# Optimization experiments

Hardware: AMD Instinct MI355X
Metric: run time of the kernel (lower is better)

The kernel has to match this reference:

```python
import jax, jax.numpy as jnp
import numpy as np
import math

N, E, B, T = 100000, 500000, 4096, 12
IN, HID, H = 64, 32, 4
HC = HID * H  # 128
ED = 4


def setup_inputs() -> dict:
    key = jax.random.key(0)
    ks = jax.random.split(key, 40)
    w = lambda k, shape: jax.random.normal(k, shape, jnp.float32) * 0.05
    inp = {
        'x': jax.random.normal(ks[0], (N, IN), jnp.float32),
        'edge_index': jax.random.randint(ks[1], (2, E), 0, N, jnp.int32),
        'edge_attr': jax.random.normal(ks[2], (E, ED), jnp.float32),
        'batch': jnp.sort(jax.random.randint(ks[3], (N,), 0, B, jnp.int32)),
        'r_target': jax.random.randint(ks[4], (B,), 0, T, jnp.int32),
        # layer 1 (in=IN)
        'Wq1': w(ks[5], (IN, HC)), 'bq1': w(ks[6], (HC,)),
        'Wk1': w(ks[7], (IN, HC)), 'bk1': w(ks[8], (HC,)),
        'Wv1': w(ks[9], (IN, HC)), 'bv1': w(ks[10], (HC,)),
        'We1': w(ks[11], (ED, HC)),
        'Ws1': w(ks[12], (IN, HC)), 'bs1': w(ks[13], (HC,)),
        # layers 2 and 3 stacked (in=HC)
        'Wq23': w(ks[14], (2, HC, HC)), 'bq23': w(ks[15], (2, HC)),
        'Wk23': w(ks[16], (2, HC, HC)), 'bk23': w(ks[17], (2, HC)),
        'Wv23': w(ks[18], (2, HC, HC)), 'bv23': w(ks[19], (2, HC)),
        'We23': w(ks[20], (2, ED, HC)),
        'Ws23': w(ks[21], (2, HC, HC)), 'bs23': w(ks[22], (2, HC)),
        # per-task linear heads (out_channels=1)
        'head_W': w(ks[23], (T, HC)), 'head_b': w(ks[24], (T,)),
    }
    return inp


def tconv(x, src, dst, ea, Wq, bq, Wk, bk, Wv, bv, We, Ws, bs):
    """PyG TransformerConv: gather -> per-edge MHA score -> segment softmax -> scatter."""
    q = (x @ Wq + bq).reshape(-1, H, HID)   # [N,H,C]
    k = (x @ Wk + bk).reshape(-1, H, HID)
    v = (x @ Wv + bv).reshape(-1, H, HID)
    e = (ea @ We).reshape(-1, H, HID)       # [E,H,C] (lin_edge has no bias)
    kj = k[src] + e                          # [E,H,C]
    alpha = (q[dst] * kj).sum(-1) / math.sqrt(HID)          # [E,H]
    amax = jax.ops.segment_max(alpha, dst, num_segments=N)  # [N,H]
    alpha = jnp.exp(alpha - amax[dst])
    asum = jax.ops.segment_sum(alpha, dst, num_segments=N)
    alpha = alpha / (asum[dst] + 1e-16)
    msg = (v[src] + e) * alpha[..., None]                   # [E,H,C]
    out = jax.ops.segment_sum(msg, dst, num_segments=N).reshape(N, HC)
    return out + x @ Ws + bs                 # root_weight skip connection


def reference(x, edge_index, edge_attr, batch, r_target,
              Wq1, bq1, Wk1, bk1, Wv1, bv1, We1, Ws1, bs1,
              Wq23, bq23, Wk23, bk23, Wv23, bv23, We23, Ws23, bs23,
              head_W, head_b):
    src, dst = edge_index[0], edge_index[1]
    h = jax.nn.relu(tconv(x, src, dst, edge_attr, Wq1, bq1, Wk1, bk1, Wv1, bv1, We1, Ws1, bs1))
    h = jax.nn.relu(tconv(h, src, dst, edge_attr, Wq23[0], bq23[0], Wk23[0], bk23[0], Wv23[0], bv23[0], We23[0], Ws23[0], bs23[0]))
    h = tconv(h, src, dst, edge_attr, Wq23[1], bq23[1], Wk23[1], bk23[1], Wv23[1], bv23[1], We23[1], Ws23[1], bs23[1])
    # global mean pool per graph
    cnt = jax.ops.segment_sum(jnp.ones((N,), h.dtype), batch, num_segments=B)
    pooled = jax.ops.segment_sum(h, batch, num_segments=B) / jnp.maximum(cnt, 1.0)[:, None]  # [B,HC]
    # dropout p=0.3 is a no-op in eval mode
    # per-task head selected by r_target (out_channels=1, squeezed)
    return (pooled * head_W[r_target]).sum(-1) + head_b[r_target]  # [B]
```

## Files before the change

### kernel.cpp

```cpp
#include <hip/hip_runtime.h>
#include <hip/hip_bf16.h>

#define NN 100000
#define EE 500000
#define BB 4096
#define HC 128
#define SCAN_ELEM 1024
#define NSB ((NN + SCAN_ELEM - 1) / SCAN_ELEM)

typedef __bf16 bf16_t;
typedef bf16_t bf16x8 __attribute__((ext_vector_type(8)));
typedef float f32x4 __attribute__((ext_vector_type(4)));
typedef float f32x2 __attribute__((ext_vector_type(2)));

__device__ __forceinline__ unsigned short f2bf(float f) {
    unsigned u = __builtin_bit_cast(unsigned, f);
    u += 0x7FFFu + ((u >> 16) & 1u);
    return (unsigned short)(u >> 16);
}
__device__ __forceinline__ float bflo(unsigned u) {
    return __builtin_bit_cast(float, u << 16);
}
__device__ __forceinline__ float bfhi(unsigned u) {
    return __builtin_bit_cast(float, u & 0xFFFF0000u);
}
__device__ __forceinline__ f32x2 unpk2(unsigned u) {
    return (f32x2){ bflo(u), bfhi(u) };
}

__global__ __launch_bounds__(256) void prep_w(
    const float* __restrict__ Wq, const float* __restrict__ Wk,
    const float* __restrict__ Wv, const float* __restrict__ Ws,
    unsigned short* __restrict__ Wt, int K)
{
    const int g = blockIdx.x * 256 + threadIdx.x;
    const int per = K * 128;
    if (g >= 4 * per) return;
    const int p = g / per, r = g - p * per;
    const int k = r >> 7, n = r & 127;
    const float* W = p == 0 ? Wq : p == 1 ? Wk : p == 2 ? Wv : Ws;
    Wt[(size_t)p * per + (size_t)n * K + k] = f2bf(W[k * 128 + n]);
}

template<int NKT, int F32A>
__global__ __launch_bounds__(256) void gemm_mfma(
    const unsigned short* __restrict__ Abf,
    const float* __restrict__ xf,
    const unsigned short* __restrict__ Wt,
    const float* __restrict__ bq, const float* __restrict__ bk,
    const float* __restrict__ bv, const float* __restrict__ bs,
    unsigned* __restrict__ QSb, unsigned* __restrict__ KVb)
{
    constexpr int K = NKT * 32;
    const int lane = threadIdx.x & 63;
    const int p = threadIdx.x >> 6;
    const int m = lane & 15, kq = lane >> 4;
    const int rows0 = blockIdx.x * 32;

    const unsigned short* Wp = Wt + (size_t)p * 128 * K;
    const float* bias = p == 0 ? bq : p == 1 ? bk : p == 2 ? bv : bs;

    bf16x8 a[2][NKT];
#pragma unroll
    for (int mt = 0; mt < 2; mt++)
#pragma unroll
        for (int kt = 0; kt < NKT; kt++) {
            if constexpr (F32A) {
                const float* pr = xf + (size_t)(rows0 + mt * 16 + m) * K + kt * 32 + kq * 8;
                const float4 f0 = *(const float4*)pr;
                const float4 f1 = *(const float4*)(pr + 4);
                union { bf16x8 v; unsigned short u8[8]; } cv;
                cv.u8[0] = f2bf(f0.x); cv.u8[1] = f2bf(f0.y);
                cv.u8[2] = f2bf(f0.z); cv.u8[3] = f2bf(f0.w);
                cv.u8[4] = f2bf(f1.x); cv.u8[5] = f2bf(f1.y);
                cv.u8[6] = f2bf(f1.z); cv.u8[7] = f2bf(f1.w);
                a[mt][kt] = cv.v;
            } else {
                a[mt][kt] = *(const bf16x8*)(Abf + (size_t)(rows0 + mt * 16 + m) * K + kt * 32 + kq * 8);
            }
        }

    f32x4 acc[2][8];
#pragma unroll
    for (int mt = 0; mt < 2; mt++)
#pragma unroll
        for (int nt = 0; nt < 8; nt++)
            acc[mt][nt] = (f32x4){0.f, 0.f, 0.f, 0.f};

#pragma unroll
    for (int nt = 0; nt < 8; nt++) {
#pragma unroll
        for (int kt = 0; kt < NKT; kt++) {
            const bf16x8 b = *(const bf16x8*)(Wp + (size_t)(nt * 16 + m) * K + kt * 32 + kq * 8);
            acc[0][nt] = __builtin_amdgcn_mfma_f32_16x16x32_bf16(a[0][kt], b, acc[0][nt], 0, 0, 0);
            acc[1][nt] = __builtin_amdgcn_mfma_f32_16x16x32_bf16(a[1][kt], b, acc[1][nt], 0, 0, 0);
        }
    }

    unsigned* out = p == 0 ? QSb : p == 1 ? KVb : p == 2 ? (KVb + 64) : (QSb + 64);
#pragma unroll
    for (int nt = 0; nt < 8; nt++) {
        const float bi = bias[nt * 16 + m];
#pragma unroll
        for (int mt = 0; mt < 2; mt++) {
#pragma unroll
            for (int r = 0; r < 4; r++) {
                const float v0 = acc[mt][nt][r] + bi;
                const float v1 = __shfl_xor(v0, 1);
                if (!(m & 1)) {
                    const unsigned pk = (unsigned)f2bf(v0) | ((unsigned)f2bf(v1) << 16);
                    out[(size_t)(rows0 + mt * 16 + kq * 4 + r) * 128 + nt * 8 + (m >> 1)] = pk;
                }
            }
        }
    }
}

__global__ __launch_bounds__(256) void deg_k(const int* __restrict__ ei, int* __restrict__ deg)
{
    const int e = blockIdx.x * 256 + threadIdx.x;
    if (e < EE) atomicAdd(&deg[ei[EE + e]], 1);
}

__global__ __launch_bounds__(256) void scan_part(const int* __restrict__ deg,
                                                 int* __restrict__ bsum)
{
    __shared__ int red[256];
    const int base = blockIdx.x * SCAN_ELEM + threadIdx.x * 4;
    int s = 0;
#pragma unroll
    for (int j = 0; j < 4; j++) { const int i = base + j; if (i < NN) s += deg[i]; }
    red[threadIdx.x] = s;
    __syncthreads();
    for (int st = 128; st > 0; st >>= 1) {
        if (threadIdx.x < st) red[threadIdx.x] += red[threadIdx.x + st];
        __syncthreads();
    }
    if (threadIdx.x == 0) bsum[blockIdx.x] = red[0];
}

__global__ __launch_bounds__(128) void scan_top(const int* __restrict__ bsum,
                                                int* __restrict__ boff)
{
    __shared__ int buf[128];
    const int v = (threadIdx.x < NSB) ? bsum[threadIdx.x] : 0;
    buf[threadIdx.x] = v;
    __syncthreads();
    for (int s = 1; s < 128; s <<= 1) {
        const int t = (threadIdx.x >= s) ? buf[threadIdx.x - s] : 0;
        __syncthreads();
        buf[threadIdx.x] += t;
        __syncthreads();
    }
    if (threadIdx.x < NSB) boff[threadIdx.x] = buf[threadIdx.x] - v;
}

__global__ __launch_bounds__(256) void scan_final(const int* __restrict__ deg,
                                                  const int* __restrict__ boff,
                                                  int* __restrict__ off,
                                                  int* __restrict__ cursor)
{
    __shared__ int tsum[256];
    const int base = blockIdx.x * SCAN_ELEM + threadIdx.x * 4;
    int vals[4];
    int s = 0;
#pragma unroll
    for (int j = 0; j < 4; j++) {
        const int i = base + j;
        vals[j] = (i < NN) ? deg[i] : 0;
        s += vals[j];
    }
    tsum[threadIdx.x] = s;
    __syncthreads();
    for (int st = 1; st < 256; st <<= 1) {
        const int t = (threadIdx.x >= st) ? tsum[threadIdx.x - st] : 0;
        __syncthreads();
        tsum[threadIdx.x] += t;
        __syncthreads();
    }
    int ex = boff[blockIdx.x] + tsum[threadIdx.x] - s;
#pragma unroll
    for (int j = 0; j < 4; j++) {
        const int i = base + j;
        if (i < NN) { off[i] = ex; cursor[i] = ex; }
        ex += vals[j];
    }
    if (blockIdx.x == NSB - 1 && threadIdx.x == 255)
        off[NN] = boff[blockIdx.x] + tsum[255];
}

__global__ __launch_bounds__(256) void bucket_k(const int* __restrict__ ei,
                                                const float* __restrict__ ea,
                                                int* __restrict__ cursor,
                                                int* __restrict__ esrc,
                                                float4* __restrict__ eaf)
{
    const int e = blockIdx.x * 256 + threadIdx.x;
    if (e < EE) {
        const int d = ei[EE + e];
        const int p = atomicAdd(&cursor[d], 1);
        esrc[p] = ei[e];
        eaf[p] = *(const float4*)(ea + (size_t)e * 4);
    }
}

__global__ __launch_bounds__(256) void cnt_k(const int* __restrict__ batch,
                                             float* __restrict__ cnt)
{
    const int n = blockIdx.x * 256 + threadIdx.x;
    if (n < NN) atomicAdd(&cnt[batch[n]], 1.0f);
}

__global__ __launch_bounds__(256) void edge_fused(
    const int* __restrict__ esrc, const float4* __restrict__ eaf,
    const float* __restrict__ We,
    const unsigned* __restrict__ QSb, const unsigned* __restrict__ KVb,
    const int* __restrict__ off,
    unsigned short* __restrict__ Hb,
    const int* __restrict__ batch, float* __restrict__ pooled,
    int fuse_pool)
{
    const int lane = threadIdx.x & 63;
    const int slot = lane >> 4;
    const int c8   = lane & 15;
    const int cb   = c8 * 8;
    const int ceq  = cb + slot * 2;
    const int n = blockIdx.x * 4 + (threadIdx.x >> 6);

    const int beg = off[n], end = off[n + 1];

    const uint4 qv = *(const uint4*)(QSb + (size_t)n * 128 + c8 * 4);
    const unsigned sku = QSb[(size_t)n * 128 + 64 + c8 * 4 + slot];
    f32x2 q2[4];
    q2[0] = unpk2(qv.x); q2[1] = unpk2(qv.y);
    q2[2] = unpk2(qv.z); q2[3] = unpk2(qv.w);

    float qep[4];
#pragma unroll
    for (int d = 0; d < 4; d++) {
        const float4 wa = *(const float4*)(We + d * HC + cb);
        const float4 wb = *(const float4*)(We + d * HC + cb + 4);
        qep[d] = wa.x * q2[0].x + wa.y * q2[0].y + wa.z * q2[1].x + wa.w * q2[1].y
               + wb.x * q2[2].x + wb.y * q2[2].y + wb.z * q2[3].x + wb.w * q2[3].y;
    }

    f32x2 num2[4] = {(f32x2){0.f, 0.f}, (f32x2){0.f, 0.f},
                     (f32x2){0.f, 0.f}, (f32x2){0.f, 0.f}};
    f32x4 s4 = (f32x4){0.f, 0.f, 0.f, 0.f};
    float den = 0.f;

    if (beg < end) {
        const int e1 = end - 1;
        int p0 = beg + slot; if (p0 > e1) p0 = e1;
        int src = esrc[p0];
        float4 a4 = eaf[p0];
        for (int base = beg; base < end; base += 4) {
            const unsigned* kv = KVb + (size_t)src * 128 + c8 * 4;
            const uint4 ku = *(const uint4*)kv;
            const uint4 vu = *(const uint4*)(kv + 64);
            const float4 ac = a4;
            const bool act = (base + slot) < end;
            if (base + 4 < end) {
                int pn = base + 4 + slot; if (pn > e1) pn = e1;
                src = esrc[pn]; a4 = eaf[pn];
            }
            f32x2 t2 = q2[0] * unpk2(ku.x);
            t2 += q2[1] * unpk2(ku.y);
            t2 += q2[2] * unpk2(ku.z);
            t2 += q2[3] * unpk2(ku.w);
            float tot = t2.x + t2.y
                      + ac.x * qep[0] + ac.y * qep[1] + ac.z * qep[2] + ac.w * qep[3];
            tot += __shfl_xor(tot, 1);
            tot += __shfl_xor(tot, 2);
            float al = __expf(tot * 0.17677669529663687f);
            if (!act) al = 0.f;
            num2[0] += unpk2(vu.x) * al;
            num2[1] += unpk2(vu.y) * al;
            num2[2] += unpk2(vu.z) * al;
            num2[3] += unpk2(vu.w) * al;
            s4.x += ac.x * al; s4.y += ac.y * al;
            s4.z += ac.z * al; s4.w += ac.w * al;
            den += al;
        }
    }

#pragma unroll
    for (int j = 0; j < 4; j++) {
        num2[j].x += __shfl_xor(num2[j].x, 16);
        num2[j].y += __shfl_xor(num2[j].y, 16);
        num2[j].x += __shfl_xor(num2[j].x, 32);
        num2[j].y += __shfl_xor(num2[j].y, 32);
    }
    s4.x += __shfl_xor(s4.x, 16); s4.y += __shfl_xor(s4.y, 16);
    s4.z += __shfl_xor(s4.z, 16); s4.w += __shfl_xor(s4.w, 16);
    s4.x += __shfl_xor(s4.x, 32); s4.y += __shfl_xor(s4.y, 32);
    s4.z += __shfl_xor(s4.z, 32); s4.w += __shfl_xor(s4.w, 32);
    den += __shfl_xor(den, 16);
    den += __shfl_xor(den, 32);
    const float inv = 1.f / (den + 1e-16f);

    f32x2 mynum = slot == 0 ? num2[0] : slot == 1 ? num2[1]
                : slot == 2 ? num2[2] : num2[3];
    float ev0 = 0.f, ev1 = 0.f;
#pragma unroll
    for (int d = 0; d < 4; d++) {
        const float2 wd = *(const float2*)(We + d * HC + ceq);
        const float sd = d == 0 ? s4.x : d == 1 ? s4.y : d == 2 ? s4.z : s4.w;
        ev0 += sd * wd.x;
        ev1 += sd * wd.y;
    }
    const float o0 = (mynum.x + ev0) * inv + bflo(sku);
    const float o1 = (mynum.y + ev1) * inv + bfhi(sku);

    if (!fuse_pool) {
        const float r0 = fmaxf(o0, 0.f), r1 = fmaxf(o1, 0.f);
        const unsigned pk = (unsigned)f2bf(r0) | ((unsigned)f2bf(r1) << 16);
        *(unsigned*)(Hb + (size_t)n * HC + ceq) = pk;
    } else {
        const int b = batch[n];
        atomicAdd(pooled + (size_t)b * HC + ceq,     o0);
        atomicAdd(pooled + (size_t)b * HC + ceq + 1, o1);
    }
}

__global__ __launch_bounds__(256) void head_k(
    const float* __restrict__ pooled, const float* __restrict__ cnt,
    const int* __restrict__ rt, const float* __restrict__ hW,
    const float* __restrict__ hb, float* __restrict__ out)
{
    const int lane = threadIdx.x & 63;
    const int b = blockIdx.x * 4 + (threadIdx.x >> 6);
    if (b >= BB) return;
    const int t = rt[b];
    const int c = lane * 2;
    const float2 p2 = *(const float2*)(pooled + (size_t)b * HC + c);
    const float2 w2 = *(const float2*)(hW + (size_t)t * HC + c);
    float part = p2.x * w2.x + p2.y * w2.y;
    part += __shfl_xor(part, 1);
    part += __shfl_xor(part, 2);
    part += __shfl_xor(part, 4);
    part += __shfl_xor(part, 8);
    part += __shfl_xor(part, 16);
    part += __shfl_xor(part, 32);
    if (lane == 0) out[b] = part / fmaxf(cnt[b], 1.0f) + hb[t];
}

extern "C" void kernel_launch(void* const* d_in, const int* in_sizes, int n_in,
                              void* d_out, int out_size, void* d_ws, size_t ws_size,
                              hipStream_t stream) {
    const float* x      = (const float*)d_in[0];
    const int*   ei     = (const int*)d_in[1];
    const float* ea     = (const float*)d_in[2];
    const int*   batch  = (const int*)d_in[3];
    const int*   rt     = (const int*)d_in[4];

    unsigned* QSb = (unsigned*)d_ws;
    unsigned* KVb = QSb + 12800000;
    unsigned short* Abf = (unsigned short*)(KVb + 12800000);
    float4* eaf   = (float4*)(Abf + 12800000);
    unsigned short* Wt = (unsigned short*)(eaf + 500000);
    float* pooled = (float*)(Wt + 65536);
    float* cnt    = pooled + 524288;
    int*   esrc   = (int*)(cnt + 4096);
    int*   deg    = esrc + 500000;
    int*   off    = deg + 100000;
    int*   cursor = off + 100004;
    int*   bsum   = cursor + 100000;
    int*   boff   = bsum + 128;

    hipMemsetAsync(deg, 0, 100000 * sizeof(int), stream);
    deg_k<<<(EE + 255) / 256, 256, 0, stream>>>(ei, deg);
    scan_part<<<NSB, 256, 0, stream>>>(deg, bsum);
    scan_top<<<1, 128, 0, stream>>>(bsum, boff);
    scan_final<<<NSB, 256, 0, stream>>>(deg, boff, off, cursor);
    bucket_k<<<(EE + 255) / 256, 256, 0, stream>>>(ei, ea, cursor, esrc, eaf);

    hipMemsetAsync(pooled, 0, (size_t)(BB * HC + BB) * sizeof(float), stream);
    cnt_k<<<(NN + 255) / 256, 256, 0, stream>>>(batch, cnt);

    for (int l = 0; l < 3; l++) {
        const int K = (l == 0) ? 64 : 128;
        const float *Wq, *Wk, *Wv, *Wsk, *bq, *bk, *bv, *bs, *We;
        if (l == 0) {
            Wq = (const float*)d_in[5];  bq = (const float*)d_in[6];
            Wk = (const float*)d_in[7];  bk = (const float*)d_in[8];
            Wv = (const float*)d_in[9];  bv = (const float*)d_in[10];
            We = (const float*)d_in[11];
            Wsk= (const float*)d_in[12]; bs = (const float*)d_in[13];
        } else {
            const int j = l - 1;
            Wq = (const float*)d_in[14] + (size_t)j * HC * HC;  bq = (const float*)d_in[15] + j * HC;
            Wk = (const float*)d_in[16] + (size_t)j * HC * HC;  bk = (const float*)d_in[17] + j * HC;
            Wv = (const float*)d_in[18] + (size_t)j * HC * HC;  bv = (const float*)d_in[19] + j * HC;
            We = (const float*)d_in[20] + (size_t)j * 4 * HC;
            Wsk= (const float*)d_in[21] + (size_t)j * HC * HC;  bs = (const float*)d_in[22] + j * HC;
        }

        prep_w<<<(4 * K * 128 + 255) / 256, 256, 0, stream>>>(Wq, Wk, Wv, Wsk, Wt, K);
        if (K == 64)
            gemm_mfma<2, 1><<<NN / 32, 256, 0, stream>>>(Abf, x, Wt, bq, bk, bv, bs, QSb, KVb);
        else
            gemm_mfma<4, 0><<<NN / 32, 256, 0, stream>>>(Abf, x, Wt, bq, bk, bv, bs, QSb, KVb);
        edge_fused<<<NN / 4, 256, 0, stream>>>(esrc, eaf, We, QSb, KVb, off,
                                               Abf, batch, pooled,
                                               l == 2 ? 1 : 0);
    }

    head_k<<<BB / 4, 256, 0, stream>>>(pooled, cnt, rt,
        (const float*)d_in[23], (const float*)d_in[24], (float*)d_out);
}
```

Before: 664.6 us.

## Batch weight prep, fold count kernel into scan, use packed bf16 converts and nontemporal stores

Converts all three layers' weights to bf16 in one launch instead of one launch per layer. Folds the per-graph node count into scan_final and merges the two memsets into one, so fewer kernels and memsets are launched. Replaces the manual bf16 rounding with the v_cvt_pk_bf16_f32 packed-convert instruction, and writes the GEMM and layer outputs with nontemporal stores. The nontemporal stores may hurt the next kernel, which reads those outputs back soon after.

```diff
diff --git a/kernel.cpp b/kernel.cpp
--- a/kernel.cpp
+++ b/kernel.cpp
@@ -27,19 +27,36 @@
 __device__ __forceinline__ f32x2 unpk2(unsigned u) {
     return (f32x2){ bflo(u), bfhi(u) };
 }
-
-__global__ __launch_bounds__(256) void prep_w(
-    const float* __restrict__ Wq, const float* __restrict__ Wk,
-    const float* __restrict__ Wv, const float* __restrict__ Ws,
-    unsigned short* __restrict__ Wt, int K)
+__device__ __forceinline__ unsigned pkbf(float lo, float hi) {
+    unsigned r;
+    asm volatile("v_cvt_pk_bf16_f32 %0, %1, %2" : "=v"(r) : "v"(lo), "v"(hi));
+    return r;
+}
+
+__global__ __launch_bounds__(256) void prep_w_all(
+    const float* __restrict__ Wq1, const float* __restrict__ Wk1,
+    const float* __restrict__ Wv1, const float* __restrict__ Ws1,
+    const float* __restrict__ Wq23, const float* __restrict__ Wk23,
+    const float* __restrict__ Wv23, const float* __restrict__ Ws23,
+    unsigned short* __restrict__ Wt3)
 {
     const int g = blockIdx.x * 256 + threadIdx.x;
-    const int per = K * 128;
-    if (g >= 4 * per) return;
-    const int p = g / per, r = g - p * per;
-    const int k = r >> 7, n = r & 127;
-    const float* W = p == 0 ? Wq : p == 1 ? Wk : p == 2 ? Wv : Ws;
-    Wt[(size_t)p * per + (size_t)n * K + k] = f2bf(W[k * 128 + n]);
+    if (g >= 32768 + 131072) return;
+    if (g < 32768) {
+        const int p = g >> 13, r = g & 8191;
+        const int k = r >> 7, n = r & 127;
+        const float* W = p == 0 ? Wq1 : p == 1 ? Wk1 : p == 2 ? Wv1 : Ws1;
+        Wt3[p * 8192 + n * 64 + k] = f2bf(W[k * 128 + n]);
+    } else {
+        const int g2 = g - 32768;
+        const int j = g2 >> 16;
+        const int r3 = g2 & 65535;
+        const int p = r3 >> 14, r = r3 & 16383;
+        const int k = r >> 7, n = r & 127;
+        const float* W = (p == 0 ? Wq23 : p == 1 ? Wk23 : p == 2 ? Wv23 : Ws23)
+                       + (size_t)j * 128 * 128;
+        Wt3[65536 + j * 65536 + p * 16384 + n * 128 + k] = f2bf(W[k * 128 + n]);
+    }
 }
 
 template<int NKT, int F32A>
@@ -69,11 +86,11 @@
                 const float* pr = xf + (size_t)(rows0 + mt * 16 + m) * K + kt * 32 + kq * 8;
                 const float4 f0 = *(const float4*)pr;
                 const float4 f1 = *(const float4*)(pr + 4);
-                union { bf16x8 v; unsigned short u8[8]; } cv;
-                cv.u8[0] = f2bf(f0.x); cv.u8[1] = f2bf(f0.y);
-                cv.u8[2] = f2bf(f0.z); cv.u8[3] = f2bf(f0.w);
-                cv.u8[4] = f2bf(f1.x); cv.u8[5] = f2bf(f1.y);
-                cv.u8[6] = f2bf(f1.z); cv.u8[7] = f2bf(f1.w);
+                union { bf16x8 v; unsigned u[4]; } cv;
+                cv.u[0] = pkbf(f0.x, f0.y);
+                cv.u[1] = pkbf(f0.z, f0.w);
+                cv.u[2] = pkbf(f1.x, f1.y);
+                cv.u[3] = pkbf(f1.z, f1.w);
                 a[mt][kt] = cv.v;
             } else {
                 a[mt][kt] = *(const bf16x8*)(Abf + (size_t)(rows0 + mt * 16 + m) * K + kt * 32 + kq * 8);
@@ -108,8 +125,9 @@
                 const float v0 = acc[mt][nt][r] + bi;
                 const float v1 = __shfl_xor(v0, 1);
                 if (!(m & 1)) {
-                    const unsigned pk = (unsigned)f2bf(v0) | ((unsigned)f2bf(v1) << 16);
-                    out[(size_t)(rows0 + mt * 16 + kq * 4 + r) * 128 + nt * 8 + (m >> 1)] = pk;
+                    const unsigned pk = pkbf(v0, v1);
+                    __builtin_nontemporal_store(pk,
+                        &out[(size_t)(rows0 + mt * 16 + kq * 4 + r) * 128 + nt * 8 + (m >> 1)]);
                 }
             }
         }
@@ -158,7 +176,9 @@
 __global__ __launch_bounds__(256) void scan_final(const int* __restrict__ deg,
                                                   const int* __restrict__ boff,
                                                   int* __restrict__ off,
-                                                  int* __restrict__ cursor)
+                                                  int* __restrict__ cursor,
+                                                  const int* __restrict__ batch,
+                                                  float* __restrict__ cnt)
 {
     __shared__ int tsum[256];
     const int base = blockIdx.x * SCAN_ELEM + threadIdx.x * 4;
@@ -182,7 +202,10 @@
 #pragma unroll
     for (int j = 0; j < 4; j++) {
         const int i = base + j;
-        if (i < NN) { off[i] = ex; cursor[i] = ex; }
+        if (i < NN) {
+            off[i] = ex; cursor[i] = ex;
+            atomicAdd(&cnt[batch[i]], 1.0f);
+        }
         ex += vals[j];
     }
     if (blockIdx.x == NSB - 1 && threadIdx.x == 255)
@@ -202,13 +225,6 @@
         esrc[p] = ei[e];
         eaf[p] = *(const float4*)(ea + (size_t)e * 4);
     }
-}
-
-__global__ __launch_bounds__(256) void cnt_k(const int* __restrict__ batch,
-                                             float* __restrict__ cnt)
-{
-    const int n = blockIdx.x * 256 + threadIdx.x;
-    if (n < NN) atomicAdd(&cnt[batch[n]], 1.0f);
 }
 
 __global__ __launch_bounds__(256) void edge_fused(
@@ -313,9 +329,8 @@
     const float o1 = (mynum.y + ev1) * inv + bfhi(sku);
 
     if (!fuse_pool) {
-        const float r0 = fmaxf(o0, 0.f), r1 = fmaxf(o1, 0.f);
-        const unsigned pk = (unsigned)f2bf(r0) | ((unsigned)f2bf(r1) << 16);
-        *(unsigned*)(Hb + (size_t)n * HC + ceq) = pk;
+        const unsigned pk = pkbf(fmaxf(o0, 0.f), fmaxf(o1, 0.f));
+        __builtin_nontemporal_store(pk, (unsigned*)(Hb + (size_t)n * HC + ceq));
     } else {
         const int b = batch[n];
         atomicAdd(pooled + (size_t)b * HC + ceq,     o0);
@@ -358,46 +373,47 @@
     unsigned* KVb = QSb + 12800000;
     unsigned short* Abf = (unsigned short*)(KVb + 12800000);
     float4* eaf   = (float4*)(Abf + 12800000);
-    unsigned short* Wt = (unsigned short*)(eaf + 500000);
-    float* pooled = (float*)(Wt + 65536);
+    unsigned short* Wt3 = (unsigned short*)(eaf + 500000);
+    float* pooled = (float*)(Wt3 + 196608);
     float* cnt    = pooled + 524288;
-    int*   esrc   = (int*)(cnt + 4096);
-    int*   deg    = esrc + 500000;
-    int*   off    = deg + 100000;
+    int*   deg    = (int*)(cnt + 4096);
+    int*   esrc   = deg + 100000;
+    int*   off    = esrc + 500000;
     int*   cursor = off + 100004;
     int*   bsum   = cursor + 100000;
     int*   boff   = bsum + 128;
 
-    hipMemsetAsync(deg, 0, 100000 * sizeof(int), stream);
+    hipMemsetAsync(pooled, 0, (size_t)(524288 + 4096 + 100000) * sizeof(float), stream);
+
     deg_k<<<(EE + 255) / 256, 256, 0, stream>>>(ei, deg);
     scan_part<<<NSB, 256, 0, stream>>>(deg, bsum);
     scan_top<<<1, 128, 0, stream>>>(bsum, boff);
-    scan_final<<<NSB, 256, 0, stream>>>(deg, boff, off, cursor);
+    scan_final<<<NSB, 256, 0, stream>>>(deg, boff, off, cursor, batch, cnt);
     bucket_k<<<(EE + 255) / 256, 256, 0, stream>>>(ei, ea, cursor, esrc, eaf);
 
-    hipMemsetAsync(pooled, 0, (size_t)(BB * HC + BB) * sizeof(float), stream);
-    cnt_k<<<(NN + 255) / 256, 256, 0, stream>>>(batch, cnt);
+    prep_w_all<<<640, 256, 0, stream>>>(
+        (const float*)d_in[5], (const float*)d_in[7], (const float*)d_in[9],
+        (const float*)d_in[12],
+        (const float*)d_in[14], (const float*)d_in[16], (const float*)d_in[18],
+        (const float*)d_in[21], Wt3);
 
     for (int l = 0; l < 3; l++) {
-        const int K = (l == 0) ? 64 : 128;
-        const float *Wq, *Wk, *Wv, *Wsk, *bq, *bk, *bv, *bs, *We;
+        const float *bq, *bk, *bv, *bs, *We;
         if (l == 0) {
-            Wq = (const float*)d_in[5];  bq = (const float*)d_in[6];
-            Wk = (const float*)d_in[7];  bk = (const float*)d_in[8];
-            Wv = (const float*)d_in[9];  bv = (const float*)d_in[10];
+            bq = (const float*)d_in[6];  bk = (const float*)d_in[8];
+            bv = (const float*)d_in[10]; bs = (const float*)d_in[13];
             We = (const float*)d_in[11];
-            Wsk= (const float*)d_in[12]; bs = (const float*)d_in[13];
         } else {
             const int j = l - 1;
-            Wq = (const float*)d_in[14] + (size_t)j * HC * HC;  bq = (const float*)d_in[15] + j * HC;
-            Wk = (const float*)d_in[16] + (size_t)j * HC * HC;  bk = (const float*)d_in[17] + j * HC;
-            Wv = (const float*)d_in[18] + (size_t)j * HC * HC;  bv = (const float*)d_in[19] + j * HC;
+            bq = (const float*)d_in[15] + j * HC;
+            bk = (const float*)d_in[17] + j * HC;
+            bv = (const float*)d_in[19] + j * HC;
+            bs = (const float*)d_in[22] + j * HC;
             We = (const float*)d_in[20] + (size_t)j * 4 * HC;
-            Wsk= (const float*)d_in[21] + (size_t)j * HC * HC;  bs = (const float*)d_in[22] + j * HC;
-        }
-
-        prep_w<<<(4 * K * 128 + 255) / 256, 256, 0, stream>>>(Wq, Wk, Wv, Wsk, Wt, K);
-        if (K == 64)
+        }
+        const unsigned short* Wt = Wt3 + (size_t)l * 65536;
+
+        if (l == 0)
             gemm_mfma<2, 1><<<NN / 32, 256, 0, stream>>>(Abf, x, Wt, bq, bk, bv, bs, QSb, KVb);
         else
             gemm_mfma<4, 0><<<NN / 32, 256, 0, stream>>>(Abf, x, Wt, bq, bk, bv, bs, QSb, KVb);
```

New measurement: 792.4 us. +19.2%, slower.
